# Kernel optimization log

Hardware: AMD Instinct MI355X
Metric: run time of the kernel (lower is better)

The kernel has to match this reference:

```python
import jax, jax.numpy as jnp
import numpy as np

B, H, W = 4, 768, 768
K = 4096            # max zero-crossing points kept per sample (padded/masked)
UPDATE_SCALE = 1.0
DIST_THRESHOLD = 3.0
W_INJECT = 1.0
W_PIXEL = 1.0
EPS = 1e-8
BIG = 1e30          # stand-in for +inf distance of invalid gt points


def _make_sdf(radius, center, key):
    # signed distance to a circle + smooth low-frequency perturbation -> realistic SDF
    r = jnp.arange(H, dtype=jnp.float32)[:, None]
    c = jnp.arange(W, dtype=jnp.float32)[None, :]
    d = jnp.sqrt((r - center[0]) ** 2 + (c - center[1]) ** 2) - radius
    noise = jax.random.normal(key, (H // 32, W // 32), dtype=jnp.float32)
    noise = jax.image.resize(noise, (H, W), method='bilinear') * 2.0
    return d + noise


def setup_inputs() -> dict:
    key = jax.random.key(0)
    ks = jax.random.split(key, 2 * B)
    preds, gts = [], []
    for b in range(B):
        cr, cc = H / 2 + 10 * b, W / 2 - 7 * b
        preds.append(_make_sdf(240.0 + 3 * b, (cr, cc), ks[2 * b]))
        gts.append(_make_sdf(250.0 - 2 * b, (cr + 5, cc - 4), ks[2 * b + 1]))
    return {"pred_sdf": jnp.stack(preds), "gt_sdf": jnp.stack(gts)}


def extract_zc(sdf):
    """Padded zero-crossing extraction: returns (K,2) coords and (K,) valid mask."""
    v1, v2 = sdf[:-1, :], sdf[1:, :]
    mask_v = (v1 * v2) < 0
    alpha_v = jnp.abs(v1) / (jnp.abs(v1) + jnp.abs(v2) + EPS)
    rs_v = jnp.arange(H - 1, dtype=jnp.float32)[:, None] + alpha_v          # (H-1,W)
    cs_v = jnp.broadcast_to(jnp.arange(W, dtype=jnp.float32)[None, :], (H - 1, W))

    h1, h2 = sdf[:, :-1], sdf[:, 1:]
    mask_h = (h1 * h2) < 0
    alpha_h = jnp.abs(h1) / (jnp.abs(h1) + jnp.abs(h2) + EPS)
    rs_h = jnp.broadcast_to(jnp.arange(H, dtype=jnp.float32)[:, None], (H, W - 1))
    cs_h = jnp.arange(W - 1, dtype=jnp.float32)[None, :] + alpha_h          # (H,W-1)

    mask_z = sdf == 0
    rz = jnp.broadcast_to(jnp.arange(H, dtype=jnp.float32)[:, None], (H, W))
    cz = jnp.broadcast_to(jnp.arange(W, dtype=jnp.float32)[None, :], (H, W))

    pts = jnp.concatenate([
        jnp.stack([rz.ravel(), cz.ravel()], -1),
        jnp.stack([rs_v.ravel(), cs_v.ravel()], -1),
        jnp.stack([rs_h.ravel(), cs_h.ravel()], -1)], axis=0)               # (M,2)
    mask = jnp.concatenate([mask_z.ravel(), mask_v.ravel(), mask_h.ravel()])
    order = jnp.argsort(~mask)[:K]      # stable sort -> True (crossing) entries first
    return pts[order], mask[order]


def compute_normals(sdf):
    gr = jnp.zeros_like(sdf)
    gr = gr.at[1:-1].set(0.5 * (sdf[2:] - sdf[:-2]))
    gr = gr.at[0].set(sdf[1] - sdf[0]).at[-1].set(sdf[-1] - sdf[-2])
    gc = jnp.zeros_like(sdf)
    gc = gc.at[:, 1:-1].set(0.5 * (sdf[:, 2:] - sdf[:, :-2]))
    gc = gc.at[:, 0].set(sdf[:, 1] - sdf[:, 0]).at[:, -1].set(sdf[:, -1] - sdf[:, -2])
    return jnp.stack([gr, gc], -1)      # (H,W,2)


def _corner(coords):
    r, c = coords[:, 0], coords[:, 1]
    r0 = jnp.clip(jnp.floor(r).astype(jnp.int32), 0, H - 1)
    c0 = jnp.clip(jnp.floor(c).astype(jnp.int32), 0, W - 1)
    r1 = jnp.clip(r0 + 1, 0, H - 1)
    c1 = jnp.clip(c0 + 1, 0, W - 1)
    ar = r - r0.astype(jnp.float32)
    ac = c - c0.astype(jnp.float32)
    return r0, c0, r1, c1, ar, ac


def bilinear_sample(img, coords):
    r0, c0, r1, c1, ar, ac = _corner(coords)
    return (img[r0, c0] * (1 - ar) * (1 - ac) + img[r0, c1] * (1 - ar) * ac
            + img[r1, c0] * ar * (1 - ac) + img[r1, c1] * ar * ac)


def chamfer_grad(pred2d, pred_zc, valid_p, gt_zc, valid_g):
    normals = compute_normals(pred2d)
    r0, c0, r1, c1, ar, ac = _corner(pred_zc)
    n = (normals[r0, c0] * ((1 - ar) * (1 - ac))[:, None]
         + normals[r0, c1] * ((1 - ar) * ac)[:, None]
         + normals[r1, c0] * (ar * (1 - ac))[:, None]
         + normals[r1, c1] * (ar * ac)[:, None])
    n = n / (jnp.linalg.norm(n, axis=1, keepdims=True) + 1e-8)

    diff = gt_zc[None, :, :] - pred_zc[:, None, :]          # (Kp,Kg,2)
    dist = jnp.linalg.norm(diff, axis=-1)                   # (Kp,Kg)
    dist = jnp.where(valid_g[None, :], dist, BIG)
    idx = jnp.argmin(dist, axis=1)
    min_dist = jnp.take_along_axis(dist, idx[:, None], 1)[:, 0]
    mask = (min_dist <= DIST_THRESHOLD) & valid_p & jnp.any(valid_g)
    dir_vec = jnp.take_along_axis(diff, idx[:, None, None], 1)[:, 0, :]
    dot = (dir_vec * n).sum(1) * UPDATE_SCALE
    dot = jnp.where(mask, dot, 0.0)

    w00 = (1 - ar) * (1 - ac); w01 = (1 - ar) * ac
    w10 = ar * (1 - ac);       w11 = ar * ac
    flat = lambda rr, cc: rr * W + cc
    indices = jnp.concatenate([flat(r0, c0), flat(r0, c1), flat(r1, c0), flat(r1, c1)])
    contribs = jnp.concatenate([dot * w00, dot * w01, dot * w10, dot * w11])
    dflat = jnp.zeros(H * W, dtype=pred2d.dtype).at[indices].add(contribs)
    return dflat.reshape(H, W)


def _per_sample(pred2d, gt2d):
    gt_zc, valid_g = extract_zc(gt2d)
    # torch uses pred.detach() for zero-crossing locations
    pred_zc, valid_p = extract_zc(jax.lax.stop_gradient(pred2d))
    dSDF = chamfer_grad(pred2d, pred_zc, valid_p, gt_zc, valid_g)
    inject = jnp.sum(pred2d * jax.lax.stop_gradient(dSDF))
    pixel = jnp.sum(jnp.where(valid_p, bilinear_sample(pred2d, pred_zc), 0.0))
    return inject, pixel


def reference(pred_sdf, gt_sdf):
    inject, pixel = jax.vmap(_per_sample)(pred_sdf, gt_sdf)
    return W_INJECT * inject.mean() + W_PIXEL * pixel.mean()
```

## Files before the change

### kernel.cpp

```cpp
#include <hip/hip_runtime.h>
#include <climits>


typedef unsigned long long ull;

constexpr int B = 4, H = 768, W = 768, K = 4096;
constexpr int HW = H * W;
constexpr int NFIELD = 2 * B;
constexpr int BANDS = 256;
constexpr int WPR = W / 64;
constexpr int SEGW = 768 * WPR;
constexpr int MSTRIDE = 3 * SEGW;
constexpr int GSPLIT = 16;
constexpr int GRNG = K / GSPLIT;
constexpr int NDBLK = B * HW / 256;

constexpr size_t OFF_ACC   = 0;
constexpr size_t OFF_CNT   = OFF_ACC + sizeof(double) * 8;
constexpr size_t OFF_WCNT  = OFF_CNT + sizeof(int) * NFIELD;
constexpr size_t OFF_MASKS = (OFF_WCNT + sizeof(int) * NFIELD * 768 + 7) & ~size_t(7);
constexpr size_t OFF_PTS   = OFF_MASKS + sizeof(ull) * NFIELD * MSTRIDE;
constexpr size_t OFF_PART  = OFF_PTS + sizeof(float2) * NFIELD * K;
constexpr size_t OFF_HEADS = OFF_PART + sizeof(ull) * (size_t)B * GSPLIT * K;
constexpr size_t OFF_NXT   = OFF_HEADS + sizeof(int) * (size_t)B * HW;
constexpr size_t OFF_EVAL  = OFF_NXT + sizeof(int) * (size_t)B * 4 * K;
constexpr size_t OFF_DIRTY = OFF_EVAL + sizeof(float) * (size_t)B * 4 * K;
constexpr size_t WS_NEED   = OFF_DIRTY + sizeof(int) * NDBLK;

#define DEVFN __device__ __forceinline__

DEVFN float grad_r(const float* __restrict__ s, int r, int c) {
#pragma clang fp contract(off)
  if (r == 0)      return s[W + c] - s[c];
  if (r == H - 1)  return s[(H - 1) * W + c] - s[(H - 2) * W + c];
  return 0.5f * (s[(r + 1) * W + c] - s[(r - 1) * W + c]);
}
DEVFN float grad_c(const float* __restrict__ s, int r, int c) {
#pragma clang fp contract(off)
  if (c == 0)      return s[r * W + 1] - s[r * W];
  if (c == W - 1)  return s[r * W + W - 1] - s[r * W + W - 2];
  return 0.5f * (s[r * W + c + 1] - s[r * W + c - 1]);
}

DEVFN const float* field_sdf(const float* pred, const float* gt, int f) {
  return ((f & 1) ? gt : pred) + (size_t)(f >> 1) * HW;
}

__global__ __launch_bounds__(256) void k_count(const float* __restrict__ pred,
                                               const float* __restrict__ gt,
                                               ull* __restrict__ masks,
                                               int* __restrict__ wave_cnt,
                                               int* __restrict__ heads,
                                               int* __restrict__ dirty,
                                               double* __restrict__ acc) {
#pragma clang fp contract(off)
  int gtid = blockIdx.x * 256 + (int)threadIdx.x;
  for (int idx = gtid; idx < B * HW; idx += gridDim.x * 256) heads[idx] = -1;
  for (int idx = gtid; idx < NDBLK; idx += gridDim.x * 256) dirty[idx] = 0;
  if (gtid < 8) acc[gtid] = 0.0;

  int f = blockIdx.x >> 6;
  int bb = blockIdx.x & 63;
  int wave = threadIdx.x >> 6, lane = threadIdx.x & 63;
  int band = bb * 4 + wave;
  int r0 = band * 3;
  const float* sdf = field_sdf(pred, gt, f);
  ull* mz = masks + (size_t)f * MSTRIDE;
  ull* mv = mz + SEGW;
  ull* mh = mv + SEGW;

  float cur[WPR], nxt[WPR];
#pragma unroll
  for (int i = 0; i < WPR; ++i) cur[i] = sdf[r0 * W + i * 64 + lane];
  int cz = 0, cv = 0, ch = 0;
  for (int rr = 0; rr < 3; ++rr) {
    int row = r0 + rr;
    bool hasNext = row < H - 1;
    if (hasNext) {
#pragma unroll
      for (int i = 0; i < WPR; ++i) nxt[i] = sdf[(row + 1) * W + i * 64 + lane];
    }
#pragma unroll
    for (int i = 0; i < WPR; ++i) {
      ull m = __ballot(cur[i] == 0.0f);
      if (lane == 0) mz[row * WPR + i] = m;
      cz += __popcll(m);
      float nb = __shfl_down(cur[i], 1);
      float nb2 = (i < WPR - 1) ? __shfl(cur[i + 1], 0) : 0.0f;
      if (lane == 63) nb = nb2;
      bool hp = (i * 64 + lane < W - 1) && (cur[i] * nb < 0.0f);
      m = __ballot(hp);
      if (lane == 0) mh[row * WPR + i] = m;
      ch += __popcll(m);
      if (hasNext) {
        m = __ballot(cur[i] * nxt[i] < 0.0f);
        if (lane == 0) mv[row * WPR + i] = m;
        cv += __popcll(m);
      }
    }
    if (hasNext) {
#pragma unroll
      for (int i = 0; i < WPR; ++i) cur[i] = nxt[i];
    }
  }
  if (lane == 0) {
    int* wc = wave_cnt + f * 768;
    wc[0 * BANDS + band] = cz;
    wc[1 * BANDS + band] = cv;
    wc[2 * BANDS + band] = ch;
  }
}

__global__ __launch_bounds__(256) void k_emit(const float* __restrict__ pred,
                                              const float* __restrict__ gt,
                                              const ull* __restrict__ masks,
                                              const int* __restrict__ wave_cnt,
                                              float2* __restrict__ pts,
                                              int* __restrict__ counts_raw) {
#pragma clang fp contract(off)
  int f = blockIdx.x / 192;
  int tb = blockIdx.x - f * 192;
  __shared__ int cnt_s[768];
  for (int t = threadIdx.x; t < 768; t += 256) cnt_s[t] = wave_cnt[f * 768 + t];
  __syncthreads();
  int wave = threadIdx.x >> 6, lane = threadIdx.x & 63;
  int task = tb * 4 + wave;
  int seg = task >> 8, band = task & 255;
  int a = 0;
  for (int idx = lane; idx < task; idx += 64) a += cnt_s[idx];
  for (int off = 32; off > 0; off >>= 1) a += __shfl_xor(a, off, 64);
  int base = a;
  if (tb == 0 && wave == 0) {
    int t2 = 0;
    for (int idx = lane; idx < 768; idx += 64) t2 += cnt_s[idx];
    for (int off = 32; off > 0; off >>= 1) t2 += __shfl_xor(t2, off, 64);
    if (lane == 0) counts_raw[f] = t2;
  }
  if (base >= K) return;
  const float* sdf = field_sdf(pred, gt, f);
  const ull* mseg = masks + (size_t)f * MSTRIDE + (size_t)seg * SEGW;
  float2* fp = pts + (size_t)f * K;
  int r0 = band * 3;
  for (int rr = 0; rr < 3; ++rr) {
    int row = r0 + rr;
    if (seg == 1 && row >= H - 1) break;
    for (int i = 0; i < WPR; ++i) {
      ull m = mseg[row * WPR + i];
      if (!m) continue;
      if ((m >> lane) & 1ull) {
        int c = i * 64 + lane;
        float pr, pc;
        if (seg == 0) {
          pr = (float)row; pc = (float)c;
        } else if (seg == 1) {
          float v1 = sdf[row * W + c], v2 = sdf[(row + 1) * W + c];
          float a1 = fabsf(v1), a2 = fabsf(v2);
          float alpha = a1 / ((a1 + a2) + 1e-8f);
          pr = (float)row + alpha; pc = (float)c;
        } else {
          float h1 = sdf[row * W + c], h2 = sdf[row * W + c + 1];
          float a1 = fabsf(h1), a2 = fabsf(h2);
          float alpha = a1 / ((a1 + a2) + 1e-8f);
          pr = (float)row; pc = (float)c + alpha;
        }
        int pos = base + __popcll(m & ((1ull << lane) - 1ull));
        if (pos < K) fp[pos] = make_float2(pr, pc);
      }
      base += __popcll(m);
      if (base >= K) { rr = 3; break; }
    }
  }
}

__global__ __launch_bounds__(256) void k_nn(const float2* __restrict__ pts,
                                            const int* __restrict__ counts_raw,
                                            ull* __restrict__ part) {
#pragma clang fp contract(off)
  int b = blockIdx.x / (16 * GSPLIT);
  int rem = blockIdx.x - b * (16 * GSPLIT);
  int ib = rem / GSPLIT, ig = rem - ib * GSPLIT;
  int np_ = min(counts_raw[2 * b + 0], K);
  int ng  = min(counts_raw[2 * b + 1], K);
  int j0 = ig * GRNG, j1 = min(j0 + GRNG, ng);
  int n = j1 - j0;
  const float2* gp = pts + (size_t)(2 * b + 1) * K;
  __shared__ float2 tile[GRNG];
  __shared__ float smin[256], smax[256];
  float rmin = __builtin_inff(), rmax = -__builtin_inff();
  for (int t = threadIdx.x; t < n; t += 256) {
    float2 g = gp[j0 + t];
    tile[t] = g;
    rmin = fminf(rmin, g.x);
    rmax = fmaxf(rmax, g.x);
  }
  smin[threadIdx.x] = rmin; smax[threadIdx.x] = rmax;
  __syncthreads();
  for (int s = 128; s > 0; s >>= 1) {
    if ((int)threadIdx.x < s) {
      smin[threadIdx.x] = fminf(smin[threadIdx.x], smin[threadIdx.x + s]);
      smax[threadIdx.x] = fmaxf(smax[threadIdx.x], smax[threadIdx.x + s]);
    }
    __syncthreads();
  }
  float gmin = smin[0] - 3.001f, gmax = smax[0] + 3.001f;

  int i = ib * 256 + (int)threadIdx.x;
  bool active = (i < np_);
  float best = __builtin_inff();
  unsigned bj = 0xffffffffu;
  if (active && n > 0) {
    float2 q = pts[(size_t)(2 * b) * K + i];
    float pr = q.x, pc = q.y;
    if (pr >= gmin && pr <= gmax) {
#pragma unroll 4
      for (int j = 0; j < n; ++j) {
        float dr = tile[j].x - pr;
        float dc = tile[j].y - pc;
        float sqf = fmaf(dr, dr, dc * dc);
        if (sqf <= 9.0001f) {
          float d = sqrtf((dr * dr) + (dc * dc));
          if (d < best) { best = d; bj = (unsigned)(j0 + j); }
        }
      }
    }
  }
  ull key = active ? (((ull)__float_as_uint(best) << 32) | bj) : ~0ull;
  part[((size_t)b * GSPLIT + ig) * K + i] = key;
}

__global__ __launch_bounds__(256) void k_post(const float* __restrict__ pred,
                                              const float2* __restrict__ pts,
                                              const int* __restrict__ counts_raw,
                                              const ull* __restrict__ part,
                                              int* __restrict__ heads,
                                              int* __restrict__ nxt,
                                              float* __restrict__ eval,
                                              int* __restrict__ dirty,
                                              double* __restrict__ acc) {
#pragma clang fp contract(off)
  int b = blockIdx.x >> 4;
  int i = ((blockIdx.x & 15) << 8) + (int)threadIdx.x;
  const float* P = pred + (size_t)b * HW;
  int np_ = min(counts_raw[2 * b + 0], K);
  bool active = (i < np_);
  float sval = 0.0f;
  if (active) {
    ull key = ~0ull;
    for (int s = 0; s < GSPLIT; ++s) {
      ull k2 = part[((size_t)b * GSPLIT + s) * K + i];
      key = k2 < key ? k2 : key;
    }
    float2 q = pts[(size_t)(2 * b) * K + i];
    float pr = q.x, pc = q.y;

    int r0 = (int)floorf(pr); r0 = r0 < 0 ? 0 : (r0 > H - 1 ? H - 1 : r0);
    int c0 = (int)floorf(pc); c0 = c0 < 0 ? 0 : (c0 > W - 1 ? W - 1 : c0);
    int r1 = (r0 + 1 > H - 1) ? H - 1 : r0 + 1;
    int c1 = (c0 + 1 > W - 1) ? W - 1 : c0 + 1;
    float ar = pr - (float)r0;
    float ac = pc - (float)c0;
    float omr = 1.0f - ar, omc = 1.0f - ac;
    float u00 = omr * omc, u01 = omr * ac, u10 = ar * omc, u11 = ar * ac;

    float v00 = P[r0 * W + c0], v01 = P[r0 * W + c1];
    float v10 = P[r1 * W + c0], v11 = P[r1 * W + c1];
    sval = (v00 * omr) * omc + (v01 * omr) * ac + (v10 * ar) * omc + (v11 * ar) * ac;

    float best = __uint_as_float((unsigned)(key >> 32));
    if (best <= 3.0f) {
      const float2* gp = pts + (size_t)(2 * b + 1) * K;
      float2 g = gp[(unsigned)(key & 0xffffffffu)];
      float grA = grad_r(P, r0, c0), grB = grad_r(P, r0, c1);
      float grC = grad_r(P, r1, c0), grD = grad_r(P, r1, c1);
      float gcA = grad_c(P, r0, c0), gcB = grad_c(P, r0, c1);
      float gcC = grad_c(P, r1, c0), gcD = grad_c(P, r1, c1);
      float n_r = ((grA * u00 + grB * u01) + grC * u10) + grD * u11;
      float n_c = ((gcA * u00 + gcB * u01) + gcC * u10) + gcD * u11;
      float nn = sqrtf((n_r * n_r) + (n_c * n_c));
      float den = nn + 1e-8f;
      float nrm_r = n_r / den, nrm_c = n_c / den;
      float dr = g.x - pr, dc = g.y - pc;
      float dot = (dr * nrm_r) + (dc * nrm_c);
      dot = dot * 1.0f;
      if (dot != 0.0f) {
        int px[4] = { r0 * W + c0, r0 * W + c1, r1 * W + c0, r1 * W + c1 };
        float cv[4] = { dot * u00, dot * u01, dot * u10, dot * u11 };
        int basee = b * 4 * K;
        for (int k2 = 0; k2 < 4; ++k2) {
          int e = k2 * K + i;
          eval[basee + e] = cv[k2];
          nxt[basee + e] = atomicExch(&heads[(size_t)b * HW + px[k2]], e);
          dirty[(b * HW + px[k2]) >> 8] = 1;
        }
      }
    }
  }
  __shared__ double red[256];
  red[threadIdx.x] = (double)sval;
  __syncthreads();
  for (int s = 128; s > 0; s >>= 1) {
    if ((int)threadIdx.x < s) red[threadIdx.x] += red[threadIdx.x + s];
    __syncthreads();
  }
  if (threadIdx.x == 0 && red[0] != 0.0) atomicAdd(&acc[4 + b], red[0]);
}

__global__ __launch_bounds__(256) void k_gather(const float* __restrict__ pred,
                                                const int* __restrict__ heads,
                                                const int* __restrict__ nxt,
                                                const float* __restrict__ eval,
                                                const int* __restrict__ dirty,
                                                double* __restrict__ acc) {
#pragma clang fp contract(off)
  if (!dirty[blockIdx.x]) return;
  int idx = blockIdx.x * 256 + (int)threadIdx.x;
  int b = idx / HW;
  float term = 0.0f;
  int h = heads[idx];
  if (h >= 0) {
    int base = b * 4 * K;
    float facc = 0.0f;
    int last = -1;
    for (;;) {
      int bestE = INT_MAX;
      for (int e = h; e >= 0; e = nxt[base + e])
        if (e > last && e < bestE) bestE = e;
      if (bestE == INT_MAX) break;
      facc = facc + eval[base + bestE];
      last = bestE;
    }
    term = pred[idx] * facc;
  }
  __shared__ double red[256];
  red[threadIdx.x] = (double)term;
  __syncthreads();
  for (int s = 128; s > 0; s >>= 1) {
    if ((int)threadIdx.x < s) red[threadIdx.x] += red[threadIdx.x + s];
    __syncthreads();
  }
  if (threadIdx.x == 0 && red[0] != 0.0)
    atomicAdd(&acc[blockIdx.x * 256 / HW], red[0]);
}

__global__ void k_final(const double* __restrict__ acc, float* __restrict__ out) {
  if (threadIdx.x == 0 && blockIdx.x == 0) {
    double mi = (acc[0] + acc[1] + acc[2] + acc[3]) * 0.25;
    double mp = (acc[4] + acc[5] + acc[6] + acc[7]) * 0.25;
    out[0] = (float)(mi + mp);
  }
}

extern "C" void kernel_launch(void* const* d_in, const int* in_sizes, int n_in,
                              void* d_out, int out_size, void* d_ws, size_t ws_size,
                              hipStream_t stream) {
  const float* pred = (const float*)d_in[0];
  const float* gt   = (const float*)d_in[1];
  float* out = (float*)d_out;
  char* ws = (char*)d_ws;

  double* acc        = (double*)(ws + OFF_ACC);
  int*    counts_raw = (int*)(ws + OFF_CNT);
  int*    wave_cnt   = (int*)(ws + OFF_WCNT);
  ull*    masks      = (ull*)(ws + OFF_MASKS);
  float2* pts        = (float2*)(ws + OFF_PTS);
  ull*    part       = (ull*)(ws + OFF_PART);
  int*    heads      = (int*)(ws + OFF_HEADS);
  int*    nxt        = (int*)(ws + OFF_NXT);
  float*  eval       = (float*)(ws + OFF_EVAL);
  int*    dirty      = (int*)(ws + OFF_DIRTY);

  (void)in_sizes; (void)n_in; (void)out_size; (void)ws_size;

  k_count<<<dim3(NFIELD * 64), dim3(256), 0, stream>>>(pred, gt, masks, wave_cnt,
                                                       heads, dirty, acc);
  k_emit<<<dim3(NFIELD * 192), dim3(256), 0, stream>>>(pred, gt, masks, wave_cnt,
                                                       pts, counts_raw);
  k_nn<<<dim3(B * 16 * GSPLIT), dim3(256), 0, stream>>>(pts, counts_raw, part);
  k_post<<<dim3(B * 16), dim3(256), 0, stream>>>(pred, pts, counts_raw, part,
                                                 heads, nxt, eval, dirty, acc);
  k_gather<<<dim3(NDBLK), dim3(256), 0, stream>>>(pred, heads, nxt, eval, dirty, acc);
  k_final<<<dim3(1), dim3(1), 0, stream>>>(acc, out);
}
```

Before: 89.95 us.

## Fuse NN search with post-processing and gather with final via last-block atomics

Merges the nearest-neighbour kernel and the post kernel: partial results now go through atomicMin into a single key array, and the last block per point-tile (detected with an atomic counter) does the bilinear/gradient work. It also folds the final reduction into the gather kernel using a done counter. The init loop uses int4 stores and additionally resets the new counters and keys. This removes two kernel launches and the partial-results buffer. In exchange it adds threadfences and atomic contention, and the tail work is serialized on the last-arriving blocks.

```diff
diff --git a/kernel.cpp b/kernel.cpp
--- a/kernel.cpp
+++ b/kernel.cpp
@@ -13,15 +13,20 @@
 constexpr int MSTRIDE = 3 * SEGW;
 constexpr int GSPLIT = 16;
 constexpr int GRNG = K / GSPLIT;
+constexpr int IBLK = K / 256;
 constexpr int NDBLK = B * HW / 256;
+
+constexpr size_t alignup(size_t x, size_t a) { return (x + a - 1) & ~(a - 1); }
 
 constexpr size_t OFF_ACC   = 0;
 constexpr size_t OFF_CNT   = OFF_ACC + sizeof(double) * 8;
-constexpr size_t OFF_WCNT  = OFF_CNT + sizeof(int) * NFIELD;
-constexpr size_t OFF_MASKS = (OFF_WCNT + sizeof(int) * NFIELD * 768 + 7) & ~size_t(7);
+constexpr size_t OFF_PCNT  = OFF_CNT + sizeof(int) * NFIELD;
+constexpr size_t OFF_DONE  = OFF_PCNT + sizeof(int) * B * IBLK;
+constexpr size_t OFF_WCNT  = OFF_DONE + sizeof(int) * 2;
+constexpr size_t OFF_MASKS = alignup(OFF_WCNT + sizeof(int) * NFIELD * 768, 8);
 constexpr size_t OFF_PTS   = OFF_MASKS + sizeof(ull) * NFIELD * MSTRIDE;
-constexpr size_t OFF_PART  = OFF_PTS + sizeof(float2) * NFIELD * K;
-constexpr size_t OFF_HEADS = OFF_PART + sizeof(ull) * (size_t)B * GSPLIT * K;
+constexpr size_t OFF_NNKEY = OFF_PTS + sizeof(float2) * NFIELD * K;
+constexpr size_t OFF_HEADS = alignup(OFF_NNKEY + sizeof(ull) * (size_t)B * K, 16);
 constexpr size_t OFF_NXT   = OFF_HEADS + sizeof(int) * (size_t)B * HW;
 constexpr size_t OFF_EVAL  = OFF_NXT + sizeof(int) * (size_t)B * 4 * K;
 constexpr size_t OFF_DIRTY = OFF_EVAL + sizeof(float) * (size_t)B * 4 * K;
@@ -52,11 +57,20 @@
                                                int* __restrict__ wave_cnt,
                                                int* __restrict__ heads,
                                                int* __restrict__ dirty,
+                                               ull* __restrict__ nnkey,
+                                               int* __restrict__ postcnt,
+                                               int* __restrict__ donecnt,
                                                double* __restrict__ acc) {
 #pragma clang fp contract(off)
   int gtid = blockIdx.x * 256 + (int)threadIdx.x;
-  for (int idx = gtid; idx < B * HW; idx += gridDim.x * 256) heads[idx] = -1;
-  for (int idx = gtid; idx < NDBLK; idx += gridDim.x * 256) dirty[idx] = 0;
+  int gsz = gridDim.x * 256;
+  int4* h4 = (int4*)heads;
+  for (int idx = gtid; idx < B * HW / 4; idx += gsz)
+    h4[idx] = make_int4(-1, -1, -1, -1);
+  for (int idx = gtid; idx < NDBLK; idx += gsz) dirty[idx] = 0;
+  for (int idx = gtid; idx < B * K; idx += gsz) nnkey[idx] = ~0ull;
+  if (gtid < B * IBLK) postcnt[gtid] = 0;
+  if (gtid == B * IBLK) *donecnt = 0;
   if (gtid < 8) acc[gtid] = 0.0;
 
   int f = blockIdx.x >> 6;
@@ -172,46 +186,54 @@
   }
 }
 
-__global__ __launch_bounds__(256) void k_nn(const float2* __restrict__ pts,
-                                            const int* __restrict__ counts_raw,
-                                            ull* __restrict__ part) {
-#pragma clang fp contract(off)
-  int b = blockIdx.x / (16 * GSPLIT);
-  int rem = blockIdx.x - b * (16 * GSPLIT);
-  int ib = rem / GSPLIT, ig = rem - ib * GSPLIT;
+__global__ __launch_bounds__(256) void k_nn_post(const float* __restrict__ pred,
+                                                 const float2* __restrict__ pts,
+                                                 const int* __restrict__ counts_raw,
+                                                 ull* __restrict__ nnkey,
+                                                 int* __restrict__ postcnt,
+                                                 int* __restrict__ heads,
+                                                 int* __restrict__ nxt,
+                                                 float* __restrict__ eval,
+                                                 int* __restrict__ dirty,
+                                                 double* __restrict__ acc) {
+#pragma clang fp contract(off)
+  int b = blockIdx.x >> 8;
+  int rem = blockIdx.x & 255;
+  int ib = rem >> 4, ig = rem & 15;
+  int tid = (int)threadIdx.x;
   int np_ = min(counts_raw[2 * b + 0], K);
   int ng  = min(counts_raw[2 * b + 1], K);
-  int j0 = ig * GRNG, j1 = min(j0 + GRNG, ng);
-  int n = j1 - j0;
+  int j0 = ig * GRNG;
+  int n = min(GRNG, ng - j0);
   const float2* gp = pts + (size_t)(2 * b + 1) * K;
+
   __shared__ float2 tile[GRNG];
   __shared__ float smin[256], smax[256];
   float rmin = __builtin_inff(), rmax = -__builtin_inff();
-  for (int t = threadIdx.x; t < n; t += 256) {
-    float2 g = gp[j0 + t];
-    tile[t] = g;
-    rmin = fminf(rmin, g.x);
-    rmax = fmaxf(rmax, g.x);
-  }
-  smin[threadIdx.x] = rmin; smax[threadIdx.x] = rmax;
+  if (tid < n) {
+    float2 g = gp[j0 + tid];
+    tile[tid] = g;
+    rmin = g.x; rmax = g.x;
+  }
+  smin[tid] = rmin; smax[tid] = rmax;
   __syncthreads();
   for (int s = 128; s > 0; s >>= 1) {
-    if ((int)threadIdx.x < s) {
-      smin[threadIdx.x] = fminf(smin[threadIdx.x], smin[threadIdx.x + s]);
-      smax[threadIdx.x] = fmaxf(smax[threadIdx.x], smax[threadIdx.x + s]);
+    if (tid < s) {
+      smin[tid] = fminf(smin[tid], smin[tid + s]);
+      smax[tid] = fmaxf(smax[tid], smax[tid + s]);
     }
     __syncthreads();
   }
   float gmin = smin[0] - 3.001f, gmax = smax[0] + 3.001f;
 
-  int i = ib * 256 + (int)threadIdx.x;
-  bool active = (i < np_);
-  float best = __builtin_inff();
-  unsigned bj = 0xffffffffu;
-  if (active && n > 0) {
+  int i = ib * 256 + tid;
+  ull key = ~0ull;
+  if (i < np_ && n > 0) {
     float2 q = pts[(size_t)(2 * b) * K + i];
     float pr = q.x, pc = q.y;
     if (pr >= gmin && pr <= gmax) {
+      float best = __builtin_inff();
+      unsigned bj = 0xffffffffu;
 #pragma unroll 4
       for (int j = 0; j < n; ++j) {
         float dr = tile[j].x - pr;
@@ -222,34 +244,27 @@
           if (d < best) { best = d; bj = (unsigned)(j0 + j); }
         }
       }
-    }
-  }
-  ull key = active ? (((ull)__float_as_uint(best) << 32) | bj) : ~0ull;
-  part[((size_t)b * GSPLIT + ig) * K + i] = key;
-}
-
-__global__ __launch_bounds__(256) void k_post(const float* __restrict__ pred,
-                                              const float2* __restrict__ pts,
-                                              const int* __restrict__ counts_raw,
-                                              const ull* __restrict__ part,
-                                              int* __restrict__ heads,
-                                              int* __restrict__ nxt,
-                                              float* __restrict__ eval,
-                                              int* __restrict__ dirty,
-                                              double* __restrict__ acc) {
-#pragma clang fp contract(off)
-  int b = blockIdx.x >> 4;
-  int i = ((blockIdx.x & 15) << 8) + (int)threadIdx.x;
+      if (bj != 0xffffffffu)
+        key = ((ull)__float_as_uint(best) << 32) | bj;
+    }
+  }
+  if (key != ~0ull) atomicMin(&nnkey[(size_t)b * K + i], key);
+  __syncthreads();
+  __shared__ int winner;
+  if (tid == 0) {
+    __threadfence();
+    int old = atomicAdd(&postcnt[b * IBLK + ib], 1);
+    winner = (old == GSPLIT - 1);
+  }
+  __syncthreads();
+  if (!winner) return;
+  __threadfence();
+
   const float* P = pred + (size_t)b * HW;
-  int np_ = min(counts_raw[2 * b + 0], K);
   bool active = (i < np_);
   float sval = 0.0f;
   if (active) {
-    ull key = ~0ull;
-    for (int s = 0; s < GSPLIT; ++s) {
-      ull k2 = part[((size_t)b * GSPLIT + s) * K + i];
-      key = k2 < key ? k2 : key;
-    }
+    ull kkey = ((const volatile ull*)nnkey)[(size_t)b * K + i];
     float2 q = pts[(size_t)(2 * b) * K + i];
     float pr = q.x, pc = q.y;
 
@@ -266,10 +281,9 @@
     float v10 = P[r1 * W + c0], v11 = P[r1 * W + c1];
     sval = (v00 * omr) * omc + (v01 * omr) * ac + (v10 * ar) * omc + (v11 * ar) * ac;
 
-    float best = __uint_as_float((unsigned)(key >> 32));
+    float best = __uint_as_float((unsigned)(kkey >> 32));
     if (best <= 3.0f) {
-      const float2* gp = pts + (size_t)(2 * b + 1) * K;
-      float2 g = gp[(unsigned)(key & 0xffffffffu)];
+      float2 g = gp[(unsigned)(kkey & 0xffffffffu)];
       float grA = grad_r(P, r0, c0), grB = grad_r(P, r0, c1);
       float grC = grad_r(P, r1, c0), grD = grad_r(P, r1, c1);
       float gcA = grad_c(P, r0, c0), gcB = grad_c(P, r0, c1);
@@ -296,57 +310,63 @@
     }
   }
   __shared__ double red[256];
-  red[threadIdx.x] = (double)sval;
+  red[tid] = (double)sval;
   __syncthreads();
   for (int s = 128; s > 0; s >>= 1) {
-    if ((int)threadIdx.x < s) red[threadIdx.x] += red[threadIdx.x + s];
+    if (tid < s) red[tid] += red[tid + s];
     __syncthreads();
   }
-  if (threadIdx.x == 0 && red[0] != 0.0) atomicAdd(&acc[4 + b], red[0]);
-}
-
-__global__ __launch_bounds__(256) void k_gather(const float* __restrict__ pred,
-                                                const int* __restrict__ heads,
-                                                const int* __restrict__ nxt,
-                                                const float* __restrict__ eval,
-                                                const int* __restrict__ dirty,
-                                                double* __restrict__ acc) {
-#pragma clang fp contract(off)
-  if (!dirty[blockIdx.x]) return;
-  int idx = blockIdx.x * 256 + (int)threadIdx.x;
-  int b = idx / HW;
-  float term = 0.0f;
-  int h = heads[idx];
-  if (h >= 0) {
-    int base = b * 4 * K;
-    float facc = 0.0f;
-    int last = -1;
-    for (;;) {
-      int bestE = INT_MAX;
-      for (int e = h; e >= 0; e = nxt[base + e])
-        if (e > last && e < bestE) bestE = e;
-      if (bestE == INT_MAX) break;
-      facc = facc + eval[base + bestE];
-      last = bestE;
-    }
-    term = pred[idx] * facc;
-  }
-  __shared__ double red[256];
-  red[threadIdx.x] = (double)term;
-  __syncthreads();
-  for (int s = 128; s > 0; s >>= 1) {
-    if ((int)threadIdx.x < s) red[threadIdx.x] += red[threadIdx.x + s];
+  if (tid == 0 && red[0] != 0.0) atomicAdd(&acc[4 + b], red[0]);
+}
+
+__global__ __launch_bounds__(256) void k_gather_final(const float* __restrict__ pred,
+                                                      const int* __restrict__ heads,
+                                                      const int* __restrict__ nxt,
+                                                      const float* __restrict__ eval,
+                                                      const int* __restrict__ dirty,
+                                                      int* __restrict__ donecnt,
+                                                      double* __restrict__ acc,
+                                                      float* __restrict__ out) {
+#pragma clang fp contract(off)
+  int tid = (int)threadIdx.x;
+  if (dirty[blockIdx.x]) {
+    int idx = blockIdx.x * 256 + tid;
+    int b = idx / HW;
+    float term = 0.0f;
+    int h = heads[idx];
+    if (h >= 0) {
+      int base = b * 4 * K;
+      float facc = 0.0f;
+      int last = -1;
+      for (;;) {
+        int bestE = INT_MAX;
+        for (int e = h; e >= 0; e = nxt[base + e])
+          if (e > last && e < bestE) bestE = e;
+        if (bestE == INT_MAX) break;
+        facc = facc + eval[base + bestE];
+        last = bestE;
+      }
+      term = pred[idx] * facc;
+    }
+    __shared__ double red[256];
+    red[tid] = (double)term;
     __syncthreads();
-  }
-  if (threadIdx.x == 0 && red[0] != 0.0)
-    atomicAdd(&acc[blockIdx.x * 256 / HW], red[0]);
-}
-
-__global__ void k_final(const double* __restrict__ acc, float* __restrict__ out) {
-  if (threadIdx.x == 0 && blockIdx.x == 0) {
-    double mi = (acc[0] + acc[1] + acc[2] + acc[3]) * 0.25;
-    double mp = (acc[4] + acc[5] + acc[6] + acc[7]) * 0.25;
-    out[0] = (float)(mi + mp);
+    for (int s = 128; s > 0; s >>= 1) {
+      if (tid < s) red[tid] += red[tid + s];
+      __syncthreads();
+    }
+    if (tid == 0 && red[0] != 0.0)
+      atomicAdd(&acc[blockIdx.x * 256 / HW], red[0]);
+  }
+  if (tid == 0) {
+    __threadfence();
+    int old = atomicAdd(donecnt, 1);
+    if (old == NDBLK - 1) {
+      const volatile double* va = acc;
+      double mi = (va[0] + va[1] + va[2] + va[3]) * 0.25;
+      double mp = (va[4] + va[5] + va[6] + va[7]) * 0.25;
+      out[0] = (float)(mi + mp);
+    }
   }
 }
 
@@ -360,10 +380,12 @@
 
   double* acc        = (double*)(ws + OFF_ACC);
   int*    counts_raw = (int*)(ws + OFF_CNT);
+  int*    postcnt    = (int*)(ws + OFF_PCNT);
+  int*    donecnt    = (int*)(ws + OFF_DONE);
   int*    wave_cnt   = (int*)(ws + OFF_WCNT);
   ull*    masks      = (ull*)(ws + OFF_MASKS);
   float2* pts        = (float2*)(ws + OFF_PTS);
-  ull*    part       = (ull*)(ws + OFF_PART);
+  ull*    nnkey      = (ull*)(ws + OFF_NNKEY);
   int*    heads      = (int*)(ws + OFF_HEADS);
   int*    nxt        = (int*)(ws + OFF_NXT);
   float*  eval       = (float*)(ws + OFF_EVAL);
@@ -372,12 +394,13 @@
   (void)in_sizes; (void)n_in; (void)out_size; (void)ws_size;
 
   k_count<<<dim3(NFIELD * 64), dim3(256), 0, stream>>>(pred, gt, masks, wave_cnt,
-                                                       heads, dirty, acc);
+                                                       heads, dirty, nnkey,
+                                                       postcnt, donecnt, acc);
   k_emit<<<dim3(NFIELD * 192), dim3(256), 0, stream>>>(pred, gt, masks, wave_cnt,
                                                        pts, counts_raw);
-  k_nn<<<dim3(B * 16 * GSPLIT), dim3(256), 0, stream>>>(pts, counts_raw, part);
-  k_post<<<dim3(B * 16), dim3(256), 0, stream>>>(pred, pts, counts_raw, part,
-                                                 heads, nxt, eval, dirty, acc);
-  k_gather<<<dim3(NDBLK), dim3(256), 0, stream>>>(pred, heads, nxt, eval, dirty, acc);
-  k_final<<<dim3(1), dim3(1), 0, stream>>>(acc, out);
-}
+  k_nn_post<<<dim3(B * IBLK * GSPLIT), dim3(256), 0, stream>>>(pred, pts, counts_raw,
+                                                               nnkey, postcnt, heads,
+                                                               nxt, eval, dirty, acc);
+  k_gather_final<<<dim3(NDBLK), dim3(256), 0, stream>>>(pred, heads, nxt, eval,
+                                                        dirty, donecnt, acc, out);
+}
```

Measured after the change: 231.9 us. 158% more time.

## Merge nearest-neighbour partial results with 64-bit atomicMin instead of split buffer

Applied to the files above, without the earlier changes.

The nearest-neighbour kernel used to write one key per gt-split (16 per point), which the post kernel then reduced. It now does an atomicMin on a single key per point, and only when a match within range was found. The key buffer is initialised to all-ones in the count kernel, and the heads init is vectorised to int4 stores. This cuts partial-buffer traffic and the reduction loop in exchange for global 64-bit atomics and an extra init pass.

```diff
diff --git a/kernel.cpp b/kernel.cpp
--- a/kernel.cpp
+++ b/kernel.cpp
@@ -13,15 +13,18 @@
 constexpr int MSTRIDE = 3 * SEGW;
 constexpr int GSPLIT = 16;
 constexpr int GRNG = K / GSPLIT;
+constexpr int IBLK = K / 256;
 constexpr int NDBLK = B * HW / 256;
+
+constexpr size_t alignup(size_t x, size_t a) { return (x + a - 1) & ~(a - 1); }
 
 constexpr size_t OFF_ACC   = 0;
 constexpr size_t OFF_CNT   = OFF_ACC + sizeof(double) * 8;
 constexpr size_t OFF_WCNT  = OFF_CNT + sizeof(int) * NFIELD;
-constexpr size_t OFF_MASKS = (OFF_WCNT + sizeof(int) * NFIELD * 768 + 7) & ~size_t(7);
+constexpr size_t OFF_MASKS = alignup(OFF_WCNT + sizeof(int) * NFIELD * 768, 8);
 constexpr size_t OFF_PTS   = OFF_MASKS + sizeof(ull) * NFIELD * MSTRIDE;
-constexpr size_t OFF_PART  = OFF_PTS + sizeof(float2) * NFIELD * K;
-constexpr size_t OFF_HEADS = OFF_PART + sizeof(ull) * (size_t)B * GSPLIT * K;
+constexpr size_t OFF_NNKEY = OFF_PTS + sizeof(float2) * NFIELD * K;
+constexpr size_t OFF_HEADS = alignup(OFF_NNKEY + sizeof(ull) * (size_t)B * K, 16);
 constexpr size_t OFF_NXT   = OFF_HEADS + sizeof(int) * (size_t)B * HW;
 constexpr size_t OFF_EVAL  = OFF_NXT + sizeof(int) * (size_t)B * 4 * K;
 constexpr size_t OFF_DIRTY = OFF_EVAL + sizeof(float) * (size_t)B * 4 * K;
@@ -52,11 +55,16 @@
                                                int* __restrict__ wave_cnt,
                                                int* __restrict__ heads,
                                                int* __restrict__ dirty,
+                                               ull* __restrict__ nnkey,
                                                double* __restrict__ acc) {
 #pragma clang fp contract(off)
   int gtid = blockIdx.x * 256 + (int)threadIdx.x;
-  for (int idx = gtid; idx < B * HW; idx += gridDim.x * 256) heads[idx] = -1;
-  for (int idx = gtid; idx < NDBLK; idx += gridDim.x * 256) dirty[idx] = 0;
+  int gsz = gridDim.x * 256;
+  int4* h4 = (int4*)heads;
+  for (int idx = gtid; idx < B * HW / 4; idx += gsz)
+    h4[idx] = make_int4(-1, -1, -1, -1);
+  for (int idx = gtid; idx < NDBLK; idx += gsz) dirty[idx] = 0;
+  for (int idx = gtid; idx < B * K; idx += gsz) nnkey[idx] = ~0ull;
   if (gtid < 8) acc[gtid] = 0.0;
 
   int f = blockIdx.x >> 6;
@@ -174,64 +182,63 @@
 
 __global__ __launch_bounds__(256) void k_nn(const float2* __restrict__ pts,
                                             const int* __restrict__ counts_raw,
-                                            ull* __restrict__ part) {
-#pragma clang fp contract(off)
-  int b = blockIdx.x / (16 * GSPLIT);
-  int rem = blockIdx.x - b * (16 * GSPLIT);
-  int ib = rem / GSPLIT, ig = rem - ib * GSPLIT;
+                                            ull* __restrict__ nnkey) {
+#pragma clang fp contract(off)
+  int b = blockIdx.x >> 8;
+  int rem = blockIdx.x & 255;
+  int ib = rem >> 4, ig = rem & 15;
+  int tid = (int)threadIdx.x;
   int np_ = min(counts_raw[2 * b + 0], K);
   int ng  = min(counts_raw[2 * b + 1], K);
-  int j0 = ig * GRNG, j1 = min(j0 + GRNG, ng);
-  int n = j1 - j0;
+  int j0 = ig * GRNG;
+  int n = min(GRNG, ng - j0);
   const float2* gp = pts + (size_t)(2 * b + 1) * K;
+
   __shared__ float2 tile[GRNG];
   __shared__ float smin[256], smax[256];
   float rmin = __builtin_inff(), rmax = -__builtin_inff();
-  for (int t = threadIdx.x; t < n; t += 256) {
-    float2 g = gp[j0 + t];
-    tile[t] = g;
-    rmin = fminf(rmin, g.x);
-    rmax = fmaxf(rmax, g.x);
-  }
-  smin[threadIdx.x] = rmin; smax[threadIdx.x] = rmax;
+  if (tid < n) {
+    float2 g = gp[j0 + tid];
+    tile[tid] = g;
+    rmin = g.x; rmax = g.x;
+  }
+  smin[tid] = rmin; smax[tid] = rmax;
   __syncthreads();
   for (int s = 128; s > 0; s >>= 1) {
-    if ((int)threadIdx.x < s) {
-      smin[threadIdx.x] = fminf(smin[threadIdx.x], smin[threadIdx.x + s]);
-      smax[threadIdx.x] = fmaxf(smax[threadIdx.x], smax[threadIdx.x + s]);
+    if (tid < s) {
+      smin[tid] = fminf(smin[tid], smin[tid + s]);
+      smax[tid] = fmaxf(smax[tid], smax[tid + s]);
     }
     __syncthreads();
   }
   float gmin = smin[0] - 3.001f, gmax = smax[0] + 3.001f;
 
-  int i = ib * 256 + (int)threadIdx.x;
-  bool active = (i < np_);
+  int i = ib * 256 + tid;
+  if (i >= np_ || n <= 0) return;
+  float2 q = pts[(size_t)(2 * b) * K + i];
+  float pr = q.x, pc = q.y;
+  if (pr < gmin || pr > gmax) return;
   float best = __builtin_inff();
   unsigned bj = 0xffffffffu;
-  if (active && n > 0) {
-    float2 q = pts[(size_t)(2 * b) * K + i];
-    float pr = q.x, pc = q.y;
-    if (pr >= gmin && pr <= gmax) {
 #pragma unroll 4
-      for (int j = 0; j < n; ++j) {
-        float dr = tile[j].x - pr;
-        float dc = tile[j].y - pc;
-        float sqf = fmaf(dr, dr, dc * dc);
-        if (sqf <= 9.0001f) {
-          float d = sqrtf((dr * dr) + (dc * dc));
-          if (d < best) { best = d; bj = (unsigned)(j0 + j); }
-        }
-      }
-    }
-  }
-  ull key = active ? (((ull)__float_as_uint(best) << 32) | bj) : ~0ull;
-  part[((size_t)b * GSPLIT + ig) * K + i] = key;
+  for (int j = 0; j < n; ++j) {
+    float dr = tile[j].x - pr;
+    float dc = tile[j].y - pc;
+    float sqf = fmaf(dr, dr, dc * dc);
+    if (sqf <= 9.0001f) {
+      float d = sqrtf((dr * dr) + (dc * dc));
+      if (d < best) { best = d; bj = (unsigned)(j0 + j); }
+    }
+  }
+  if (bj != 0xffffffffu)
+    atomicMin(&nnkey[(size_t)b * K + i],
+              ((ull)__float_as_uint(best) << 32) | bj);
 }
 
 __global__ __launch_bounds__(256) void k_post(const float* __restrict__ pred,
                                               const float2* __restrict__ pts,
                                               const int* __restrict__ counts_raw,
-                                              const ull* __restrict__ part,
+                                              const ull* __restrict__ nnkey,
                                               int* __restrict__ heads,
                                               int* __restrict__ nxt,
                                               float* __restrict__ eval,
@@ -245,11 +252,7 @@
   bool active = (i < np_);
   float sval = 0.0f;
   if (active) {
-    ull key = ~0ull;
-    for (int s = 0; s < GSPLIT; ++s) {
-      ull k2 = part[((size_t)b * GSPLIT + s) * K + i];
-      key = k2 < key ? k2 : key;
-    }
+    ull key = nnkey[(size_t)b * K + i];
     float2 q = pts[(size_t)(2 * b) * K + i];
     float pr = q.x, pc = q.y;
 
@@ -363,7 +366,7 @@
   int*    wave_cnt   = (int*)(ws + OFF_WCNT);
   ull*    masks      = (ull*)(ws + OFF_MASKS);
   float2* pts        = (float2*)(ws + OFF_PTS);
-  ull*    part       = (ull*)(ws + OFF_PART);
+  ull*    nnkey      = (ull*)(ws + OFF_NNKEY);
   int*    heads      = (int*)(ws + OFF_HEADS);
   int*    nxt        = (int*)(ws + OFF_NXT);
   float*  eval       = (float*)(ws + OFF_EVAL);
@@ -372,12 +375,12 @@
   (void)in_sizes; (void)n_in; (void)out_size; (void)ws_size;
 
   k_count<<<dim3(NFIELD * 64), dim3(256), 0, stream>>>(pred, gt, masks, wave_cnt,
-                                                       heads, dirty, acc);
+                                                       heads, dirty, nnkey, acc);
   k_emit<<<dim3(NFIELD * 192), dim3(256), 0, stream>>>(pred, gt, masks, wave_cnt,
                                                        pts, counts_raw);
-  k_nn<<<dim3(B * 16 * GSPLIT), dim3(256), 0, stream>>>(pts, counts_raw, part);
-  k_post<<<dim3(B * 16), dim3(256), 0, stream>>>(pred, pts, counts_raw, part,
-                                                 heads, nxt, eval, dirty, acc);
+  k_nn<<<dim3(B * IBLK * GSPLIT), dim3(256), 0, stream>>>(pts, counts_raw, nnkey);
+  k_post<<<dim3(B * IBLK), dim3(256), 0, stream>>>(pred, pts, counts_raw, nnkey,
+                                                   heads, nxt, eval, dirty, acc);
   k_gather<<<dim3(NDBLK), dim3(256), 0, stream>>>(pred, heads, nxt, eval, dirty, acc);
   k_final<<<dim3(1), dim3(1), 0, stream>>>(acc, out);
 }
```

Measured after the change: 90.31 us. No clear change (+0.4%).
